# Optimization experiments

Hardware: AMD Instinct MI355X
Metric: run time of the kernel (lower is better)

The kernel has to match this reference:

```python
import jax, jax.numpy as jnp
import numpy as np
import math

D_MODEL = 512
N_HEADS = 8
FACTOR = 5
B, L_Q, L_K = 8, 4096, 4096


def setup_inputs() -> dict:
    key = jax.random.key(0)
    ks = jax.random.split(key, 9)
    s = 0.02
    sample_k = max(1, int(FACTOR * math.log(L_K + 1)))  # 41
    return {
        "query": jax.random.normal(ks[0], (B, L_Q, D_MODEL), jnp.float32),
        "key_in": jax.random.normal(ks[1], (B, L_K, D_MODEL), jnp.float32),
        "value": jax.random.normal(ks[2], (B, L_K, D_MODEL), jnp.float32),
        "W_Q": jax.random.normal(ks[3], (D_MODEL, D_MODEL), jnp.float32) * s,
        "W_K": jax.random.normal(ks[4], (D_MODEL, D_MODEL), jnp.float32) * s,
        "W_V": jax.random.normal(ks[5], (D_MODEL, D_MODEL), jnp.float32) * s,
        "W_out": jax.random.normal(ks[6], (D_MODEL, D_MODEL), jnp.float32) * s,
        "b_out": jnp.zeros((D_MODEL,), jnp.float32),
        "sample_idx": jax.random.randint(ks[8], (L_Q, sample_k), 0, L_K),
    }


def reference(query, key_in, value, W_Q, W_K, W_V, W_out, b_out, sample_idx):
    b, lq, _ = query.shape
    lk = key_in.shape[1]
    H = N_HEADS
    E = D_MODEL // H
    # projections -> [B, H, L, E]
    Q = (query @ W_Q).reshape(b, lq, H, E).transpose(0, 2, 1, 3)
    K = (key_in @ W_K).reshape(b, lk, H, E).transpose(0, 2, 1, 3)
    V = (value @ W_V).reshape(b, lk, H, E).transpose(0, 2, 1, 3)

    u = max(1, int(FACTOR * math.log(lq + 1)))  # top-u queries (41)

    # sparsity proxy M(q_i, K) on randomly sampled keys
    K_sample = K[:, :, sample_idx, :]                      # [B,H,L_Q,S,E]
    QK_sample = jnp.einsum('bhqe,bhqse->bhqs', Q, K_sample)
    M = QK_sample.max(axis=-1) - QK_sample.mean(axis=-1)   # [B,H,L_Q]
    _, M_top = jax.lax.top_k(M, u)                         # [B,H,u]

    # attention for the top-u queries only
    Q_reduce = jnp.take_along_axis(Q, M_top[..., None], axis=2)  # [B,H,u,E]
    scale = 1.0 / math.sqrt(E)
    scores = jnp.einsum('bhue,bhke->bhuk', Q_reduce, K) * scale
    attn = jax.nn.softmax(scores, axis=-1)  # dropout is identity (eval)
    ctx_top = jnp.einsum('bhuk,bhke->bhue', attn, V)       # [B,H,u,E]

    # mean-value context for the lazy queries, scatter-update the active ones
    ctx = jnp.broadcast_to(V.mean(axis=2, keepdims=True), (b, H, lq, E))
    bi = jnp.arange(b)[:, None, None]
    hi = jnp.arange(H)[None, :, None]
    ctx = ctx.at[bi, hi, M_top].set(ctx_top)

    ctx = ctx.transpose(0, 2, 1, 3).reshape(b, lq, H * E)
    return ctx @ W_out + b_out
```

## Files before the change

kernel.cpp:

```cpp
#include <hip/hip_runtime.h>
#include <cstdint>
#include <cstddef>

#define D_MODEL 512
#define NHEADS  8
#define EDIM    64
#define BATCH   8
#define LSEQ    4096

typedef unsigned short u16;
typedef __attribute__((ext_vector_type(8))) short short8;
typedef __attribute__((ext_vector_type(4))) float f32x4;

__device__ __forceinline__ u16 bf16_rne(float x) {
  unsigned int u = __float_as_uint(x);
  u += 0x7FFFu + ((u >> 16) & 1u);
  return (u16)(u >> 16);
}
__device__ __forceinline__ void split2(float x, u16& h, u16& l) {
  h = bf16_rne(x);
  float hf = __uint_as_float((unsigned int)h << 16);
  l = bf16_rne(x - hf);
}

__global__ __launch_bounds__(256) void cvt_x(
    const float* __restrict__ X, u16* __restrict__ P, int planeStride) {
  size_t i = ((size_t)blockIdx.x * 256 + threadIdx.x) * 4;
  float4 x = *(const float4*)(X + i);
  ushort4 h, l;
  split2(x.x, h.x, l.x);
  split2(x.y, h.y, l.y);
  split2(x.z, h.z, l.z);
  split2(x.w, h.w, l.w);
  *(ushort4*)(P + i) = h;
  *(ushort4*)(P + planeStride + i) = l;
}

__global__ __launch_bounds__(256) void cvt_w(
    const float* __restrict__ W0, const float* __restrict__ W1,
    const float* __restrict__ W2, const float* __restrict__ W3,
    u16* __restrict__ out) {
  const float* W = (blockIdx.z == 0) ? W0 : ((blockIdx.z == 1) ? W1 :
                   ((blockIdx.z == 2) ? W2 : W3));
  u16* P = out + (size_t)blockIdx.z * 524288;
  __shared__ float tile[64][65];
  const int k0 = blockIdx.x * 64, n0 = blockIdx.y * 64;
  const int t = threadIdx.x;
  const int tr = t >> 4, tc = (t & 15) * 4;
#pragma unroll
  for (int j = 0; j < 4; ++j) {
    int kr = tr + j * 16;
    float4 v = *(const float4*)(W + (size_t)(k0 + kr) * 512 + n0 + tc);
    tile[kr][tc + 0] = v.x; tile[kr][tc + 1] = v.y;
    tile[kr][tc + 2] = v.z; tile[kr][tc + 3] = v.w;
  }
  __syncthreads();
#pragma unroll
  for (int j = 0; j < 4; ++j) {
    int nr = tr + j * 16;
    ushort4 h, l;
    split2(tile[tc + 0][nr], h.x, l.x);
    split2(tile[tc + 1][nr], h.y, l.y);
    split2(tile[tc + 2][nr], h.z, l.z);
    split2(tile[tc + 3][nr], h.w, l.w);
    size_t off = (size_t)(n0 + nr) * 512 + k0 + tc;
    *(ushort4*)(P + off) = h;
    *(ushort4*)(P + 262144 + off) = l;
  }
}

__device__ __forceinline__ void gld_lds16(const char* g, char* l) {
  __builtin_amdgcn_global_load_lds((const __attribute__((address_space(1))) void*)g,
                                   (__attribute__((address_space(3))) void*)l, 16, 0, 0);
}

__global__ __launch_bounds__(256, 2) void gemm_mfma(
    const u16* __restrict__ XP, int xPlaneStride,
    const u16* __restrict__ WP, float* __restrict__ Y) {
  __shared__ u16 Ah[128 * 32];
  __shared__ u16 Al[128 * 32];
  __shared__ u16 Bh[128 * 32];
  __shared__ u16 Bl[128 * 32];
  const int tid = threadIdx.x;
  const int lane = tid & 63, wv = tid >> 6;
  const int wm = (wv & 1) * 64, wn = (wv >> 1) * 64;
  const int bm = blockIdx.x * 128, bn = blockIdx.y * 128;
  const int fr = lane & 15, quad = lane >> 4;
  const int sRow = tid >> 2, sColB = (tid & 3) * 16;

  f32x4 acc[16];
#pragma unroll
  for (int i = 0; i < 16; ++i) acc[i] = (f32x4){0.f, 0.f, 0.f, 0.f};

  const u16* Xh = XP;
  const u16* Xl = XP + xPlaneStride;
  const u16* Wh = WP;
  const u16* Wl = WP + 262144;

  for (int kk = 0; kk < 16; ++kk) {
#pragma unroll
    for (int j = 0; j < 2; ++j) {
      const size_t rA = (size_t)(bm + j * 64 + sRow) * 512 + kk * 32;
      const size_t rB = (size_t)(bn + j * 64 + sRow) * 512 + kk * 32;
      const int lo = (j * 256 + wv * 64) * 16;
      gld_lds16((const char*)(Xh + rA) + sColB, (char*)Ah + lo);
      gld_lds16((const char*)(Xl + rA) + sColB, (char*)Al + lo);
      gld_lds16((const char*)(Wh + rB) + sColB, (char*)Bh + lo);
      gld_lds16((const char*)(Wl + rB) + sColB, (char*)Bl + lo);
    }
    __syncthreads();
    short8 ah[4], al[4], bh[4], bl[4];
#pragma unroll
    for (int mi = 0; mi < 4; ++mi) {
      ah[mi] = *(const short8*)&Ah[(wm + mi * 16 + fr) * 32 + quad * 8];
      al[mi] = *(const short8*)&Al[(wm + mi * 16 + fr) * 32 + quad * 8];
    }
#pragma unroll
    for (int ni = 0; ni < 4; ++ni) {
      bh[ni] = *(const short8*)&Bh[(wn + ni * 16 + fr) * 32 + quad * 8];
      bl[ni] = *(const short8*)&Bl[(wn + ni * 16 + fr) * 32 + quad * 8];
    }
#pragma unroll
    for (int mi = 0; mi < 4; ++mi)
#pragma unroll
      for (int ni = 0; ni < 4; ++ni)
        acc[mi * 4 + ni] = __builtin_amdgcn_mfma_f32_16x16x32_bf16(
            ah[mi], bh[ni], acc[mi * 4 + ni], 0, 0, 0);
#pragma unroll
    for (int mi = 0; mi < 4; ++mi)
#pragma unroll
      for (int ni = 0; ni < 4; ++ni)
        acc[mi * 4 + ni] = __builtin_amdgcn_mfma_f32_16x16x32_bf16(
            ah[mi], bl[ni], acc[mi * 4 + ni], 0, 0, 0);
#pragma unroll
    for (int mi = 0; mi < 4; ++mi)
#pragma unroll
      for (int ni = 0; ni < 4; ++ni)
        acc[mi * 4 + ni] = __builtin_amdgcn_mfma_f32_16x16x32_bf16(
            al[mi], bh[ni], acc[mi * 4 + ni], 0, 0, 0);
    __syncthreads();
  }
#pragma unroll
  for (int mi = 0; mi < 4; ++mi)
#pragma unroll
    for (int ni = 0; ni < 4; ++ni) {
      const f32x4 a = acc[mi * 4 + ni];
      float* yp = Y + (size_t)(bm + wm + mi * 16 + quad * 4) * 512 + (bn + wn + ni * 16 + fr);
#pragma unroll
      for (int r = 0; r < 4; ++r) yp[(size_t)r * 512] = a[r];
    }
}

__global__ __launch_bounds__(256) void qk_sample_half(
    const float* __restrict__ Q, const float* __restrict__ K,
    const int* __restrict__ sidx, float* __restrict__ M, int S, int hg) {
  const int blk = blockIdx.x;
  const int lane = threadIdx.x & 63;
  const int b = blk & 7;
  const int q = ((blk >> 3) << 2) + (threadIdx.x >> 6);
  const int s = lane >> 5;
  const int hl = (lane >> 3) & 3;
  const int d = lane & 7;
  const int h = hg * 4 + hl;
  const int col = hg * 256 + hl * 64 + d * 8;

  const float* Qp = Q + ((size_t)b * LSEQ + q) * D_MODEL + col;
  const float4 q0 = *(const float4*)Qp;
  const float4 q1 = *(const float4*)(Qp + 4);
  const float* Kb = K + (size_t)b * LSEQ * D_MODEL + col;
  const int* sp = sidx + (size_t)q * S;

  auto rowp = [&](int j) -> const float* {
    int jj = j + s;
    int row = sp[(jj < S) ? jj : (S - 1)];
    return Kb + (size_t)row * D_MODEL;
  };

  const float* pr0 = rowp(0);
  float4 a0 = *(const float4*)pr0, b0 = *(const float4*)(pr0 + 4);
  const float* pr1 = rowp(2);
  float4 a1 = *(const float4*)pr1, b1 = *(const float4*)(pr1 + 4);

  float mx = -3.4e38f, sum = 0.0f;
  for (int j = 0; j < S; j += 2) {
    const float4 ca = a0, cb = b0;
    a0 = a1; b0 = b1;
    const float* pn = rowp(j + 4);
    a1 = *(const float4*)pn;
    b1 = *(const float4*)(pn + 4);
    float p = ca.x * q0.x + ca.y * q0.y + ca.z * q0.z + ca.w * q0.w +
              cb.x * q1.x + cb.y * q1.y + cb.z * q1.z + cb.w * q1.w;
    p += __shfl_xor(p, 1, 64);
    p += __shfl_xor(p, 2, 64);
    p += __shfl_xor(p, 4, 64);
    if (j + s < S) {
      mx = fmaxf(mx, p);
      sum += p;
    }
  }
  mx = fmaxf(mx, __shfl_xor(mx, 32, 64));
  sum += __shfl_xor(sum, 32, 64);
  if (s == 0 && d == 0)
    M[((size_t)(b * NHEADS + h)) * LSEQ + q] = mx - sum / (float)S;
}

__global__ __launch_bounds__(256) void topk_kernel(
    const float* __restrict__ M, int* __restrict__ Mtop, int U) {
  __shared__ float vals[LSEQ];
  __shared__ float rmax[256];
  __shared__ int ridx[256];
  int bh = blockIdx.x;
  int t = threadIdx.x;
  for (int i = t; i < LSEQ; i += 256) vals[i] = M[(size_t)bh * LSEQ + i];
  __syncthreads();
  for (int it = 0; it < U; ++it) {
    float best = -3.4e38f; int bi = -1;
    for (int i = t; i < LSEQ; i += 256) {
      float v = vals[i];
      if (v > best) { best = v; bi = i; }
    }
    rmax[t] = best; ridx[t] = bi;
    __syncthreads();
    for (int s = 128; s > 0; s >>= 1) {
      if (t < s) {
        if (rmax[t + s] > rmax[t]) { rmax[t] = rmax[t + s]; ridx[t] = ridx[t + s]; }
      }
      __syncthreads();
    }
    if (t == 0) {
      Mtop[(size_t)bh * U + it] = ridx[0];
      vals[ridx[0]] = -3.4e38f;
    }
    __syncthreads();
  }
}

__global__ __launch_bounds__(256, 2) void attn_flash(
    const float* __restrict__ Q, const float* __restrict__ K,
    const float* __restrict__ V, const int* __restrict__ Mtop,
    float* __restrict__ part_ctx, float* __restrict__ part_m,
    float* __restrict__ part_l, int U, int nsplit, int chunks_per_block) {
  __shared__ u16 KhS[64 * 72];
  __shared__ u16 KlS[64 * 72];
  __shared__ float VsS[64 * 68];
  const int bh = blockIdx.y, split = blockIdx.x;
  const int h = bh & (NHEADS - 1), b = bh >> 3;
  const int t = threadIdx.x, w = t >> 6, lane = t & 63;
  const int fr = lane & 15, quad = lane >> 4;

  const int qi = w * 16 + fr;
  const int qrow = (qi < U) ? Mtop[(size_t)bh * U + qi] : Mtop[(size_t)bh * U];
  const float4* Qr = (const float4*)(Q + ((size_t)(b * LSEQ) + qrow) * D_MODEL + h * EDIM);
  float4 qa = Qr[quad * 2], qb = Qr[quad * 2 + 1];
  float4 qc = Qr[quad * 2 + 8], qd = Qr[quad * 2 + 9];
  short8 qh0, ql0, qh1, ql1;
  {
    u16 hh, ll;
    split2(qa.x, hh, ll); qh0[0] = (short)hh; ql0[0] = (short)ll;
    split2(qa.y, hh, ll); qh0[1] = (short)hh; ql0[1] = (short)ll;
    split2(qa.z, hh, ll); qh0[2] = (short)hh; ql0[2] = (short)ll;
    split2(qa.w, hh, ll); qh0[3] = (short)hh; ql0[3] = (short)ll;
    split2(qb.x, hh, ll); qh0[4] = (short)hh; ql0[4] = (short)ll;
    split2(qb.y, hh, ll); qh0[5] = (short)hh; ql0[5] = (short)ll;
    split2(qb.z, hh, ll); qh0[6] = (short)hh; ql0[6] = (short)ll;
    split2(qb.w, hh, ll); qh0[7] = (short)hh; ql0[7] = (short)ll;
    split2(qc.x, hh, ll); qh1[0] = (short)hh; ql1[0] = (short)ll;
    split2(qc.y, hh, ll); qh1[1] = (short)hh; ql1[1] = (short)ll;
    split2(qc.z, hh, ll); qh1[2] = (short)hh; ql1[2] = (short)ll;
    split2(qc.w, hh, ll); qh1[3] = (short)hh; ql1[3] = (short)ll;
    split2(qd.x, hh, ll); qh1[4] = (short)hh; ql1[4] = (short)ll;
    split2(qd.y, hh, ll); qh1[5] = (short)hh; ql1[5] = (short)ll;
    split2(qd.z, hh, ll); qh1[6] = (short)hh; ql1[6] = (short)ll;
    split2(qd.w, hh, ll); qh1[7] = (short)hh; ql1[7] = (short)ll;
  }

  float4 c4[16];
#pragma unroll
  for (int i = 0; i < 16; ++i) c4[i] = make_float4(0.f, 0.f, 0.f, 0.f);
  float m = -1e30f, l = 0.0f;

  const int r = t >> 2, cg = t & 3;

  const int k_base = split * (chunks_per_block * 64);
  for (int c = 0; c < chunks_per_block; ++c) {
    const int k0 = k_base + c * 64;
    const float4* Kg4 = (const float4*)(K + ((size_t)(b * LSEQ) + k0 + r) * D_MODEL + h * EDIM);
    const float4* Vg4 = (const float4*)(V + ((size_t)(b * LSEQ) + k0 + r) * D_MODEL + h * EDIM);
#pragma unroll
    for (int i = 0; i < 4; ++i) {
      const int f4 = cg + 4 * i;
      float4 kv = Kg4[f4];
      float4 vv = Vg4[f4];
      ushort4 hh, ll;
      split2(kv.x, hh.x, ll.x);
      split2(kv.y, hh.y, ll.y);
      split2(kv.z, hh.z, ll.z);
      split2(kv.w, hh.w, ll.w);
      *(ushort4*)&KhS[r * 72 + f4 * 4] = hh;
      *(ushort4*)&KlS[r * 72 + f4 * 4] = ll;
      *(float4*)&VsS[r * 68 + f4 * 4] = vv;
    }
    __syncthreads();

    f32x4 acc[4];
#pragma unroll
    for (int mt = 0; mt < 4; ++mt) acc[mt] = (f32x4){0.f, 0.f, 0.f, 0.f};
#pragma unroll
    for (int mt = 0; mt < 4; ++mt) {
      short8 kh = *(const short8*)&KhS[(mt * 16 + fr) * 72 + quad * 8];
      short8 kl = *(const short8*)&KlS[(mt * 16 + fr) * 72 + quad * 8];
      acc[mt] = __builtin_amdgcn_mfma_f32_16x16x32_bf16(kh, qh0, acc[mt], 0, 0, 0);
      acc[mt] = __builtin_amdgcn_mfma_f32_16x16x32_bf16(kh, ql0, acc[mt], 0, 0, 0);
      acc[mt] = __builtin_amdgcn_mfma_f32_16x16x32_bf16(kl, qh0, acc[mt], 0, 0, 0);
    }
#pragma unroll
    for (int mt = 0; mt < 4; ++mt) {
      short8 kh = *(const short8*)&KhS[(mt * 16 + fr) * 72 + 32 + quad * 8];
      short8 kl = *(const short8*)&KlS[(mt * 16 + fr) * 72 + 32 + quad * 8];
      acc[mt] = __builtin_amdgcn_mfma_f32_16x16x32_bf16(kh, qh1, acc[mt], 0, 0, 0);
      acc[mt] = __builtin_amdgcn_mfma_f32_16x16x32_bf16(kh, ql1, acc[mt], 0, 0, 0);
      acc[mt] = __builtin_amdgcn_mfma_f32_16x16x32_bf16(kl, qh1, acc[mt], 0, 0, 0);
    }

    float cm = -3.4e38f;
#pragma unroll
    for (int mt = 0; mt < 4; ++mt) {
#pragma unroll
      for (int rr = 0; rr < 4; ++rr) {
        float s = acc[mt][rr] * 0.125f;
        acc[mt][rr] = s;
        cm = fmaxf(cm, s);
      }
    }
    cm = fmaxf(cm, __shfl_xor(cm, 16, 64));
    cm = fmaxf(cm, __shfl_xor(cm, 32, 64));
    float mn = fmaxf(m, cm);
    if (mn > m) {
      float f = __expf(m - mn);
      l *= f;
#pragma unroll
      for (int i = 0; i < 16; ++i) {
        c4[i].x *= f; c4[i].y *= f; c4[i].z *= f; c4[i].w *= f;
      }
      m = mn;
    }
    float psum = 0.0f;
#pragma unroll
    for (int mt = 0; mt < 4; ++mt) {
#pragma unroll
      for (int rr = 0; rr < 4; ++rr) {
        float p = __expf(acc[mt][rr] - m);
        acc[mt][rr] = p;
        psum += p;
      }
    }
    l += psum;

#pragma unroll
    for (int mt = 0; mt < 4; ++mt) {
#pragma unroll
      for (int rr = 0; rr < 4; ++rr) {
        const int krow = mt * 16 + quad * 4 + rr;
        const float4* vr = (const float4*)&VsS[krow * 68];
        const float p = acc[mt][rr];
#pragma unroll
        for (int i = 0; i < 16; ++i) {
          float4 vv = vr[i];
          c4[i].x += p * vv.x; c4[i].y += p * vv.y;
          c4[i].z += p * vv.z; c4[i].w += p * vv.w;
        }
      }
    }
    __syncthreads();
  }

#pragma unroll
  for (int i = 0; i < 16; ++i) {
    c4[i].x += __shfl_xor(c4[i].x, 16, 64);
    c4[i].y += __shfl_xor(c4[i].y, 16, 64);
    c4[i].z += __shfl_xor(c4[i].z, 16, 64);
    c4[i].w += __shfl_xor(c4[i].w, 16, 64);
    c4[i].x += __shfl_xor(c4[i].x, 32, 64);
    c4[i].y += __shfl_xor(c4[i].y, 32, 64);
    c4[i].z += __shfl_xor(c4[i].z, 32, 64);
    c4[i].w += __shfl_xor(c4[i].w, 32, 64);
  }
  l += __shfl_xor(l, 16, 64);
  l += __shfl_xor(l, 32, 64);

  if (quad == 0 && qi < U) {
    part_m[(size_t)(bh * nsplit + split) * 64 + qi] = m;
    part_l[(size_t)(bh * nsplit + split) * 64 + qi] = l;
  }
  float* pc = part_ctx + (size_t)(bh * nsplit + split) * 4096;
  if (quad == 0) {
#pragma unroll
    for (int ii = 0; ii < 16; ++ii) pc[ii * 64 + qi] = (&c4[ii >> 2].x)[ii & 3];
  } else if (quad == 1) {
#pragma unroll
    for (int ii = 0; ii < 16; ++ii) pc[(16 + ii) * 64 + qi] = (&c4[4 + (ii >> 2)].x)[ii & 3];
  } else if (quad == 2) {
#pragma unroll
    for (int ii = 0; ii < 16; ++ii) pc[(32 + ii) * 64 + qi] = (&c4[8 + (ii >> 2)].x)[ii & 3];
  } else {
#pragma unroll
    for (int ii = 0; ii < 16; ++ii) pc[(48 + ii) * 64 + qi] = (&c4[12 + (ii >> 2)].x)[ii & 3];
  }
}

__global__ __launch_bounds__(256) void attn_combine(
    const float* __restrict__ part_ctx, const float* __restrict__ part_m,
    const float* __restrict__ part_l, float* __restrict__ ctxTop,
    int U, int nsplit) {
  __shared__ float F[16][64];
  const int bh = blockIdx.x;
  const int t = threadIdx.x, lane = t & 63, grp = t >> 6;
  if (grp == 0) {
    float M = -3.4e38f;
    for (int s = 0; s < nsplit; ++s)
      M = fmaxf(M, part_m[(size_t)(bh * nsplit + s) * 64 + lane]);
    float L = 0.0f;
    for (int s = 0; s < nsplit; ++s)
      L += part_l[(size_t)(bh * nsplit + s) * 64 + lane] *
           __expf(part_m[(size_t)(bh * nsplit + s) * 64 + lane] - M);
    float invL = 1.0f / L;
    for (int s = 0; s < nsplit; ++s)
      F[s][lane] = __expf(part_m[(size_t)(bh * nsplit + s) * 64 + lane] - M) * invL;
  }
  __syncthreads();
  for (int ei = 0; ei < 16; ++ei) {
    int e = grp * 16 + ei;
    float acc = 0.0f;
    for (int s = 0; s < nsplit; ++s)
      acc += F[s][lane] * part_ctx[(size_t)(bh * nsplit + s) * 4096 + e * 64 + lane];
    if (lane < U) ctxTop[((size_t)bh * U + lane) * 64 + e] = acc;
  }
}

__global__ __launch_bounds__(256) void vmean_kernel(
    const float* __restrict__ V, float* __restrict__ Vm) {
  __shared__ float part[4][EDIM];
  int bh = blockIdx.x;
  int h = bh & (NHEADS - 1), b = bh >> 3;
  int t = threadIdx.x;
  int e = t & 63, c = t >> 6;
  float s = 0.0f;
  for (int k = c * (LSEQ / 4); k < (c + 1) * (LSEQ / 4); ++k)
    s += V[((size_t)b * LSEQ + k) * D_MODEL + h * EDIM + e];
  part[c][e] = s;
  __syncthreads();
  if (c == 0)
    Vm[(size_t)bh * EDIM + e] =
        (part[0][e] + part[1][e] + part[2][e] + part[3][e]) * (1.0f / (float)LSEQ);
}

__global__ __launch_bounds__(256) void base_out_kernel(
    const float* __restrict__ Vm, const float* __restrict__ Wout,
    const float* __restrict__ bout, float* __restrict__ base) {
  __shared__ float cb[D_MODEL];
  int b = blockIdx.x;
  int t = threadIdx.x;
  for (int d = t; d < D_MODEL; d += 256) cb[d] = Vm[(size_t)b * D_MODEL + d];
  __syncthreads();
  for (int n = t; n < D_MODEL; n += 256) {
    float s = bout[n];
    for (int d = 0; d < D_MODEL; ++d) s += cb[d] * Wout[(size_t)d * D_MODEL + n];
    base[(size_t)b * D_MODEL + n] = s;
  }
}

__global__ __launch_bounds__(256) void fill_out(
    const float* __restrict__ base, float* __restrict__ out) {
  size_t i = (size_t)blockIdx.x * 256 + threadIdx.x;
  int n4 = (int)(i & 127);
  size_t bq = i >> 7;
  int b = (int)(bq >> 12);
  float4 v = ((const float4*)base)[(size_t)b * 128 + n4];
  ((float4*)out)[i] = v;
}

__global__ __launch_bounds__(256, 1) void delta_out_mfma(
    const float* __restrict__ ctxTop, const float* __restrict__ Vm,
    const int* __restrict__ Mtop, const u16* __restrict__ WoutTP,
    float* __restrict__ out, int U) {
  __shared__ u16 Dh[64 * 72];
  __shared__ u16 Dl[64 * 72];
  __shared__ int qr[64];
  const int bh = blockIdx.x;
  const int h = bh & (NHEADS - 1), b = bh >> 3;
  const int t = threadIdx.x, lane = t & 63, wv = t >> 6;
  const int fr = lane & 15, quad = lane >> 4;

  {
    const int r = t >> 2, c0 = (t & 3) * 16;
#pragma unroll
    for (int j = 0; j < 4; ++j) {
      float4 v = make_float4(0.f, 0.f, 0.f, 0.f);
      if (r < U) {
        float4 cv = *(const float4*)(ctxTop + ((size_t)bh * U + r) * EDIM + c0 + j * 4);
        float4 mv = *(const float4*)(Vm + (size_t)bh * EDIM + c0 + j * 4);
        v = make_float4(cv.x - mv.x, cv.y - mv.y, cv.z - mv.z, cv.w - mv.w);
      }
      ushort4 hh, ll;
      split2(v.x, hh.x, ll.x);
      split2(v.y, hh.y, ll.y);
      split2(v.z, hh.z, ll.z);
      split2(v.w, hh.w, ll.w);
      *(ushort4*)&Dh[r * 72 + c0 + j * 4] = hh;
      *(ushort4*)&Dl[r * 72 + c0 + j * 4] = ll;
    }
  }
  if (t < 64) qr[t] = (t < U) ? Mtop[(size_t)bh * U + t] : -1;
  __syncthreads();

  f32x4 acc[32];
#pragma unroll
  for (int i = 0; i < 32; ++i) acc[i] = (f32x4){0.f, 0.f, 0.f, 0.f};

  const u16* Wh = WoutTP;
  const u16* Wl = WoutTP + 262144;

#pragma unroll
  for (int ks = 0; ks < 2; ++ks) {
    short8 a_h[4], a_l[4];
#pragma unroll
    for (int mt = 0; mt < 4; ++mt) {
      a_h[mt] = *(const short8*)&Dh[(mt * 16 + fr) * 72 + ks * 32 + quad * 8];
      a_l[mt] = *(const short8*)&Dl[(mt * 16 + fr) * 72 + ks * 32 + quad * 8];
    }
#pragma unroll
    for (int nt = 0; nt < 8; ++nt) {
      const int n = wv * 128 + nt * 16 + fr;
      const size_t off = (size_t)n * 512 + h * EDIM + ks * 32 + quad * 8;
      short8 b_h = *(const short8*)&Wh[off];
      short8 b_l = *(const short8*)&Wl[off];
#pragma unroll
      for (int mt = 0; mt < 4; ++mt) {
        acc[mt * 8 + nt] = __builtin_amdgcn_mfma_f32_16x16x32_bf16(
            a_h[mt], b_h, acc[mt * 8 + nt], 0, 0, 0);
        acc[mt * 8 + nt] = __builtin_amdgcn_mfma_f32_16x16x32_bf16(
            a_h[mt], b_l, acc[mt * 8 + nt], 0, 0, 0);
        acc[mt * 8 + nt] = __builtin_amdgcn_mfma_f32_16x16x32_bf16(
            a_l[mt], b_h, acc[mt * 8 + nt], 0, 0, 0);
      }
    }
  }

  int qreg[16];
#pragma unroll
  for (int mt = 0; mt < 4; ++mt)
#pragma unroll
    for (int r4 = 0; r4 < 4; ++r4) qreg[mt * 4 + r4] = qr[mt * 16 + quad * 4 + r4];
#pragma unroll
  for (int mt = 0; mt < 4; ++mt)
#pragma unroll
    for (int nt = 0; nt < 8; ++nt) {
      const f32x4 a = acc[mt * 8 + nt];
      const int n = wv * 128 + nt * 16 + fr;
#pragma unroll
      for (int r4 = 0; r4 < 4; ++r4) {
        const int q = qreg[mt * 4 + r4];
        if (q >= 0)
          atomicAdd(out + ((size_t)b * LSEQ + q) * D_MODEL + n, a[r4]);
      }
    }
}

extern "C" void kernel_launch(void* const* d_in, const int* in_sizes, int n_in,
                              void* d_out, int out_size, void* d_ws, size_t ws_size,
                              hipStream_t stream) {
  const float* query  = (const float*)d_in[0];
  const float* key_in = (const float*)d_in[1];
  const float* value  = (const float*)d_in[2];
  const float* W_Q    = (const float*)d_in[3];
  const float* W_K    = (const float*)d_in[4];
  const float* W_V    = (const float*)d_in[5];
  const float* W_out  = (const float*)d_in[6];
  const float* b_out  = (const float*)d_in[7];
  const int*   sidx   = (const int*)d_in[8];
  float* out = (float*)d_out;

  const int S = in_sizes[8] / LSEQ;
  const int U = S;

  char* ws = (char*)d_ws;
  size_t o = 0;
  float* Qf     = (float*)(ws + o); o += (size_t)BATCH * LSEQ * D_MODEL * 4;
  float* Kf     = (float*)(ws + o); o += (size_t)BATCH * LSEQ * D_MODEL * 4;
  float* Vf     = (float*)(ws + o); o += (size_t)BATCH * LSEQ * D_MODEL * 4;
  int*   Mtop   = (int*)  (ws + o); o += ((size_t)64 * U * 4 + 255) & ~255ULL;
  float* ctxTop = (float*)(ws + o); o += ((size_t)64 * U * EDIM * 4 + 255) & ~255ULL;
  float* Vm     = (float*)(ws + o); o += 16384;
  float* baseO  = (float*)(ws + o); o += 16384;
  u16*   Wpl    = (u16*)  (ws + o); o += (size_t)4 * 524288 * 2;
  size_t unionOff = o;

  int nchunk = 1;
  while (nchunk < 16 &&
         unionOff + 2 * ((size_t)(32768 / nchunk) * 512 * 2) > ws_size)
    nchunk <<= 1;
  const int Mchunk = 32768 / nchunk;
  u16* planes = (u16*)(ws + unionOff);
  const int planeStride = Mchunk * 512;

  float* M = (float*)(ws + unionOff);
  int nsplit = 16;
  for (;;) {
    size_t need = unionOff + 2 * ((size_t)64 * nsplit * 64 * 4)
                  + (size_t)64 * nsplit * 4096 * 4;
    if (need <= ws_size || nsplit == 1) break;
    nsplit >>= 1;
  }
  float* part_m   = (float*)(ws + unionOff);
  float* part_l   = part_m + (size_t)64 * nsplit * 64;
  float* part_ctx = part_l + (size_t)64 * nsplit * 64;
  const int chunks_per_block = 64 / nsplit;

  cvt_w<<<dim3(8, 8, 4), 256, 0, stream>>>(W_Q, W_K, W_V, W_out, Wpl);
  const float* Xsrc[3] = {query, key_in, value};
  float* Ydst[3] = {Qf, Kf, Vf};
  for (int g = 0; g < 3; ++g) {
    for (int c = 0; c < nchunk; ++c) {
      const float* xc = Xsrc[g] + (size_t)c * Mchunk * 512;
      float* yc = Ydst[g] + (size_t)c * Mchunk * 512;
      cvt_x<<<(Mchunk * 512) / 1024, 256, 0, stream>>>(xc, planes, planeStride);
      gemm_mfma<<<dim3(Mchunk / 128, 4), 256, 0, stream>>>(
          planes, planeStride, Wpl + (size_t)g * 524288, yc);
    }
  }

  qk_sample_half<<<(BATCH * LSEQ) / 4, 256, 0, stream>>>(Qf, Kf, sidx, M, S, 0);
  qk_sample_half<<<(BATCH * LSEQ) / 4, 256, 0, stream>>>(Qf, Kf, sidx, M, S, 1);
  topk_kernel<<<BATCH * NHEADS, 256, 0, stream>>>(M, Mtop, U);
  attn_flash<<<dim3(nsplit, BATCH * NHEADS), 256, 0, stream>>>(
      Qf, Kf, Vf, Mtop, part_ctx, part_m, part_l, U, nsplit, chunks_per_block);
  attn_combine<<<BATCH * NHEADS, 256, 0, stream>>>(
      part_ctx, part_m, part_l, ctxTop, U, nsplit);
  vmean_kernel<<<BATCH * NHEADS, 256, 0, stream>>>(Vf, Vm);
  base_out_kernel<<<BATCH, 256, 0, stream>>>(Vm, W_out, b_out, baseO);
  fill_out<<<(BATCH * LSEQ * (D_MODEL / 4)) / 256, 256, 0, stream>>>(baseO, out);
  delta_out_mfma<<<BATCH * NHEADS, 256, 0, stream>>>(
      ctxTop, Vm, Mtop, Wpl + (size_t)3 * 524288, out, U);
}
```

Before: 843.0 us.

## Fuse fp32-to-bf16 split of activations into projection GEMM; deepen sample-key prefetch

```diff
diff --git a/kernel.cpp b/kernel.cpp
--- a/kernel.cpp
+++ b/kernel.cpp
@@ -21,19 +21,6 @@
   h = bf16_rne(x);
   float hf = __uint_as_float((unsigned int)h << 16);
   l = bf16_rne(x - hf);
-}
-
-__global__ __launch_bounds__(256) void cvt_x(
-    const float* __restrict__ X, u16* __restrict__ P, int planeStride) {
-  size_t i = ((size_t)blockIdx.x * 256 + threadIdx.x) * 4;
-  float4 x = *(const float4*)(X + i);
-  ushort4 h, l;
-  split2(x.x, h.x, l.x);
-  split2(x.y, h.y, l.y);
-  split2(x.z, h.z, l.z);
-  split2(x.w, h.w, l.w);
-  *(ushort4*)(P + i) = h;
-  *(ushort4*)(P + planeStride + i) = l;
 }
 
 __global__ __launch_bounds__(256) void cvt_w(
@@ -74,46 +61,70 @@
                                    (__attribute__((address_space(3))) void*)l, 16, 0, 0);
 }
 
-__global__ __launch_bounds__(256, 2) void gemm_mfma(
-    const u16* __restrict__ XP, int xPlaneStride,
-    const u16* __restrict__ WP, float* __restrict__ Y) {
-  __shared__ u16 Ah[128 * 32];
-  __shared__ u16 Al[128 * 32];
+__global__ __launch_bounds__(256, 2) void gemm_fused(
+    const float* __restrict__ X, const u16* __restrict__ WP,
+    float* __restrict__ Y) {
+  __shared__ u16 Ah[128 * 40];
+  __shared__ u16 Al[128 * 40];
   __shared__ u16 Bh[128 * 32];
   __shared__ u16 Bl[128 * 32];
   const int tid = threadIdx.x;
   const int lane = tid & 63, wv = tid >> 6;
   const int wm = (wv & 1) * 64, wn = (wv >> 1) * 64;
-  const int bm = blockIdx.x * 128, bn = blockIdx.y * 128;
+  const int bn = blockIdx.x * 128, bm = blockIdx.y * 128;
   const int fr = lane & 15, quad = lane >> 4;
   const int sRow = tid >> 2, sColB = (tid & 3) * 16;
+  const int ar = tid >> 1, ac = (tid & 1) * 16;
 
   f32x4 acc[16];
 #pragma unroll
   for (int i = 0; i < 16; ++i) acc[i] = (f32x4){0.f, 0.f, 0.f, 0.f};
 
-  const u16* Xh = XP;
-  const u16* Xl = XP + xPlaneStride;
   const u16* Wh = WP;
   const u16* Wl = WP + 262144;
+  const float* Arow = X + (size_t)(bm + ar) * 512 + ac;
+
+  union V8 { ushort4 v4[2]; short8 v8; };
 
   for (int kk = 0; kk < 16; ++kk) {
+    float4 x0 = *(const float4*)(Arow + kk * 32);
+    float4 x1 = *(const float4*)(Arow + kk * 32 + 4);
+    float4 x2 = *(const float4*)(Arow + kk * 32 + 8);
+    float4 x3 = *(const float4*)(Arow + kk * 32 + 12);
 #pragma unroll
     for (int j = 0; j < 2; ++j) {
-      const size_t rA = (size_t)(bm + j * 64 + sRow) * 512 + kk * 32;
       const size_t rB = (size_t)(bn + j * 64 + sRow) * 512 + kk * 32;
       const int lo = (j * 256 + wv * 64) * 16;
-      gld_lds16((const char*)(Xh + rA) + sColB, (char*)Ah + lo);
-      gld_lds16((const char*)(Xl + rA) + sColB, (char*)Al + lo);
       gld_lds16((const char*)(Wh + rB) + sColB, (char*)Bh + lo);
       gld_lds16((const char*)(Wl + rB) + sColB, (char*)Bl + lo);
     }
+    V8 h0, l0, h1, l1;
+    split2(x0.x, h0.v4[0].x, l0.v4[0].x);
+    split2(x0.y, h0.v4[0].y, l0.v4[0].y);
+    split2(x0.z, h0.v4[0].z, l0.v4[0].z);
+    split2(x0.w, h0.v4[0].w, l0.v4[0].w);
+    split2(x1.x, h0.v4[1].x, l0.v4[1].x);
+    split2(x1.y, h0.v4[1].y, l0.v4[1].y);
+    split2(x1.z, h0.v4[1].z, l0.v4[1].z);
+    split2(x1.w, h0.v4[1].w, l0.v4[1].w);
+    split2(x2.x, h1.v4[0].x, l1.v4[0].x);
+    split2(x2.y, h1.v4[0].y, l1.v4[0].y);
+    split2(x2.z, h1.v4[0].z, l1.v4[0].z);
+    split2(x2.w, h1.v4[0].w, l1.v4[0].w);
+    split2(x3.x, h1.v4[1].x, l1.v4[1].x);
+    split2(x3.y, h1.v4[1].y, l1.v4[1].y);
+    split2(x3.z, h1.v4[1].z, l1.v4[1].z);
+    split2(x3.w, h1.v4[1].w, l1.v4[1].w);
+    *(short8*)&Ah[ar * 40 + ac]     = h0.v8;
+    *(short8*)&Ah[ar * 40 + ac + 8] = h1.v8;
+    *(short8*)&Al[ar * 40 + ac]     = l0.v8;
+    *(short8*)&Al[ar * 40 + ac + 8] = l1.v8;
     __syncthreads();
     short8 ah[4], al[4], bh[4], bl[4];
 #pragma unroll
     for (int mi = 0; mi < 4; ++mi) {
-      ah[mi] = *(const short8*)&Ah[(wm + mi * 16 + fr) * 32 + quad * 8];
-      al[mi] = *(const short8*)&Al[(wm + mi * 16 + fr) * 32 + quad * 8];
+      ah[mi] = *(const short8*)&Ah[(wm + mi * 16 + fr) * 40 + quad * 8];
+      al[mi] = *(const short8*)&Al[(wm + mi * 16 + fr) * 40 + quad * 8];
     }
 #pragma unroll
     for (int ni = 0; ni < 4; ++ni) {
@@ -170,24 +181,27 @@
   const float* Kb = K + (size_t)b * LSEQ * D_MODEL + col;
   const int* sp = sidx + (size_t)q * S;
 
-  auto rowp = [&](int j) -> const float* {
+  auto spclamp = [&](int j) -> int {
     int jj = j + s;
-    int row = sp[(jj < S) ? jj : (S - 1)];
-    return Kb + (size_t)row * D_MODEL;
+    return sp[(jj < S) ? jj : (S - 1)];
   };
 
-  const float* pr0 = rowp(0);
-  float4 a0 = *(const float4*)pr0, b0 = *(const float4*)(pr0 + 4);
-  const float* pr1 = rowp(2);
-  float4 a1 = *(const float4*)pr1, b1 = *(const float4*)(pr1 + 4);
+  int i0 = spclamp(0), i1 = spclamp(2), i2 = spclamp(4), i3 = spclamp(6);
+  const float* p0 = Kb + (size_t)i0 * D_MODEL;
+  float4 a0 = *(const float4*)p0, b0 = *(const float4*)(p0 + 4);
+  const float* p1 = Kb + (size_t)i1 * D_MODEL;
+  float4 a1 = *(const float4*)p1, b1 = *(const float4*)(p1 + 4);
+  const float* p2 = Kb + (size_t)i2 * D_MODEL;
+  float4 a2 = *(const float4*)p2, b2 = *(const float4*)(p2 + 4);
 
   float mx = -3.4e38f, sum = 0.0f;
   for (int j = 0; j < S; j += 2) {
     const float4 ca = a0, cb = b0;
-    a0 = a1; b0 = b1;
-    const float* pn = rowp(j + 4);
-    a1 = *(const float4*)pn;
-    b1 = *(const float4*)(pn + 4);
+    a0 = a1; b0 = b1; a1 = a2; b1 = b2;
+    const float* pn = Kb + (size_t)i3 * D_MODEL;
+    a2 = *(const float4*)pn;
+    b2 = *(const float4*)(pn + 4);
+    i3 = spclamp(j + 8);
     float p = ca.x * q0.x + ca.y * q0.y + ca.z * q0.z + ca.w * q0.w +
               cb.x * q1.x + cb.y * q1.y + cb.z * q1.z + cb.w * q1.w;
     p += __shfl_xor(p, 1, 64);
@@ -595,14 +609,6 @@
   u16*   Wpl    = (u16*)  (ws + o); o += (size_t)4 * 524288 * 2;
   size_t unionOff = o;
 
-  int nchunk = 1;
-  while (nchunk < 16 &&
-         unionOff + 2 * ((size_t)(32768 / nchunk) * 512 * 2) > ws_size)
-    nchunk <<= 1;
-  const int Mchunk = 32768 / nchunk;
-  u16* planes = (u16*)(ws + unionOff);
-  const int planeStride = Mchunk * 512;
-
   float* M = (float*)(ws + unionOff);
   int nsplit = 16;
   for (;;) {
@@ -617,17 +623,9 @@
   const int chunks_per_block = 64 / nsplit;
 
   cvt_w<<<dim3(8, 8, 4), 256, 0, stream>>>(W_Q, W_K, W_V, W_out, Wpl);
-  const float* Xsrc[3] = {query, key_in, value};
-  float* Ydst[3] = {Qf, Kf, Vf};
-  for (int g = 0; g < 3; ++g) {
-    for (int c = 0; c < nchunk; ++c) {
-      const float* xc = Xsrc[g] + (size_t)c * Mchunk * 512;
-      float* yc = Ydst[g] + (size_t)c * Mchunk * 512;
-      cvt_x<<<(Mchunk * 512) / 1024, 256, 0, stream>>>(xc, planes, planeStride);
-      gemm_mfma<<<dim3(Mchunk / 128, 4), 256, 0, stream>>>(
-          planes, planeStride, Wpl + (size_t)g * 524288, yc);
-    }
-  }
+  gemm_fused<<<dim3(4, 256), 256, 0, stream>>>(query,  Wpl,                       Qf);
+  gemm_fused<<<dim3(4, 256), 256, 0, stream>>>(key_in, Wpl + (size_t)1 * 524288,  Kf);
+  gemm_fused<<<dim3(4, 256), 256, 0, stream>>>(value,  Wpl + (size_t)2 * 524288,  Vf);
 
   qk_sample_half<<<(BATCH * LSEQ) / 4, 256, 0, stream>>>(Qf, Kf, sidx, M, S, 0);
   qk_sample_half<<<(BATCH * LSEQ) / 4, 256, 0, stream>>>(Qf, Kf, sidx, M, S, 1);
```

Measured after the change: 779.2 us. -7.6%, faster.
